# Performance work log

Measured on AMD Instinct MI355X. Metric: run time of the kernel, lower is better.

Reference implementation:

```python
import jax, jax.numpy as jnp
import numpy as np
import math

DMODEL = 1024
DFF = 4096
NUM_EXPERTS = 8
TOPK = 2
CAP_FACTOR = 1.25
EPS = 1.1920929e-07  # torch.finfo(float32).eps


def _trunc_normal(key, shape, fan_in, scale=1.0):
    std = scale * (1.0 / fan_in) ** 0.5
    return jax.random.truncated_normal(key, -2.0, 2.0, shape, jnp.float32) * std


def setup_inputs() -> dict:
    key = jax.random.key(0)
    ks = jax.random.split(key, 5)
    return {
        "x": jax.random.normal(ks[0], (2, 2048, DMODEL), jnp.float32),
        "router_weight": _trunc_normal(ks[1], (NUM_EXPERTS, DMODEL), DMODEL),
        "ff_pre_act_weight": _trunc_normal(ks[2], (NUM_EXPERTS, DFF, DMODEL), DMODEL),
        "gate_weight": _trunc_normal(ks[3], (NUM_EXPERTS, DFF, DMODEL), DMODEL),
        "ff_post_act_weight": _trunc_normal(ks[4], (NUM_EXPERTS, DMODEL, DFF), DFF),
    }


def reference(x, router_weight, ff_pre_act_weight, gate_weight, ff_post_act_weight):
    orig_shape = x.shape
    h = x.reshape(-1, DMODEL)                      # [T, d]
    T = h.shape[0]

    # ---- router: softmax + top-k, renormalize top-k probs ----
    logits = jnp.einsum('th,eh->te', h, router_weight)
    probs = jax.nn.softmax(logits.astype(jnp.float32), axis=-1)
    topk_probs, selected = jax.lax.top_k(probs, TOPK)          # [T,k]
    topk_probs = topk_probs / jnp.maximum(topk_probs.sum(-1, keepdims=True), EPS)

    flat_tokens = jnp.repeat(jnp.arange(T), TOPK)              # [T*k]
    flat_experts = selected.reshape(-1)
    flat_weights = topk_probs.reshape(-1)
    A = T * TOPK                                               # total assignments (static)
    capacity = max(1, math.ceil(CAP_FACTOR * A / NUM_EXPERTS))

    # ---- stable sort: by weight desc, then grouped by expert (stable) ----
    weight_order = jnp.argsort(-flat_weights, stable=True)
    grouped_order = jnp.argsort(flat_experts[weight_order], stable=True)
    sort_order = weight_order[grouped_order]
    se = flat_experts[sort_order]
    st = flat_tokens[sort_order]
    sw = flat_weights[sort_order]

    # ---- capacity dropping (mask instead of boolean filter, jit-safe) ----
    counts = jnp.bincount(se, length=NUM_EXPERTS)
    offsets = jnp.cumsum(counts) - counts
    slot = jnp.arange(A) - offsets[se]
    keep = slot < capacity
    sw = jnp.where(keep, sw, 0.0)

    # renormalize weights over kept assignments per token
    token_wsum = jnp.zeros(T, jnp.float32).at[st].add(sw)
    kept_w = sw / jnp.maximum(token_wsum[st], EPS)

    # ---- dispatch: scatter tokens into [E*capacity, d] (+1 dump row for dropped) ----
    FC = NUM_EXPERTS * capacity
    dispatch = jnp.where(keep, se * capacity + slot, FC)
    expert_inputs = jnp.zeros((FC + 1, DMODEL), x.dtype).at[dispatch].set(h[st])
    expert_inputs = expert_inputs[:FC].reshape(NUM_EXPERTS, capacity, DMODEL)

    # ---- grouped SwiGLU expert GEMMs ----
    pre = jnp.einsum('ech,edh->ecd', expert_inputs, ff_pre_act_weight)
    gate = jnp.einsum('ech,edh->ecd', expert_inputs, gate_weight)
    expert_out = jnp.einsum('ecd,ehd->ech', pre * jax.nn.silu(gate), ff_post_act_weight)

    # ---- combine: gather per-assignment output, weight, scatter-add to tokens ----
    eo_flat = jnp.concatenate(
        [expert_out.reshape(FC, DMODEL), jnp.zeros((1, DMODEL), x.dtype)], axis=0)
    updates = eo_flat[dispatch] * kept_w.astype(x.dtype)[:, None]
    out = jnp.zeros((T, DMODEL), x.dtype).at[st].add(updates)
    return out.reshape(orig_shape)
```

## Files before the change

### kernel.cpp

```cpp
#include <hip/hip_runtime.h>
#include <math.h>

#define DMODEL 1024
#define DFF    4096
#define NE     8
#define EPSF   1.1920929e-07f

typedef float f4    __attribute__((ext_vector_type(4)));
typedef float f32x4 __attribute__((ext_vector_type(4)));
typedef short s16x8 __attribute__((ext_vector_type(8)));
typedef unsigned short u16x4 __attribute__((ext_vector_type(4)));

__device__ inline unsigned short bf16_rne(float f) {
  unsigned int u = __float_as_uint(f);
  u += 0x7fffu + ((u >> 16) & 1u);
  return (unsigned short)(u >> 16);
}
__device__ inline float bf16_up(unsigned short h) {
  return __uint_as_float(((unsigned int)h) << 16);
}

__global__ void moe_init(int* __restrict__ used_count, int* __restrict__ row_tok, int n_row) {
  int i = blockIdx.x * blockDim.x + threadIdx.x;
  if (i < NE) used_count[i] = 0;
  for (int j = i; j < n_row; j += gridDim.x * blockDim.x) row_tok[j] = -1;
}

__global__ __launch_bounds__(256)
void moe_router(const float* __restrict__ x, const float* __restrict__ rw,
                int* __restrict__ assign_e, float* __restrict__ assign_w, int T) {
  int gw = (int)((blockIdx.x * blockDim.x + threadIdx.x) >> 6);
  int lane = threadIdx.x & 63;
  if (gw >= T) return;
  const float* h = x + (size_t)gw * DMODEL;
  float acc[NE];
#pragma unroll
  for (int e = 0; e < NE; ++e) acc[e] = 0.f;
  for (int i = lane; i < DMODEL; i += 64) {
    float hv = h[i];
#pragma unroll
    for (int e = 0; e < NE; ++e) acc[e] = fmaf(hv, rw[e * DMODEL + i], acc[e]);
  }
#pragma unroll
  for (int e = 0; e < NE; ++e) {
    float v = acc[e];
    for (int o = 32; o > 0; o >>= 1) v += __shfl_xor(v, o, 64);
    acc[e] = v;
  }
  if (lane == 0) {
    float mx = acc[0];
#pragma unroll
    for (int e = 1; e < NE; ++e) mx = fmaxf(mx, acc[e]);
    float p[NE];
    float s = 0.f;
#pragma unroll
    for (int e = 0; e < NE; ++e) { p[e] = expf(acc[e] - mx); s += p[e]; }
#pragma unroll
    for (int e = 0; e < NE; ++e) p[e] /= s;
    int e0 = 0;
#pragma unroll
    for (int e = 1; e < NE; ++e) if (p[e] > p[e0]) e0 = e;
    int e1 = (e0 == 0) ? 1 : 0;
#pragma unroll
    for (int e = 0; e < NE; ++e) { if (e != e0 && p[e] > p[e1]) e1 = e; }
    float w0 = p[e0], w1 = p[e1];
    float wsum = fmaxf(w0 + w1, EPSF);
    assign_e[2 * gw] = e0;
    assign_e[2 * gw + 1] = e1;
    assign_w[2 * gw] = w0 / wsum;
    assign_w[2 * gw + 1] = w1 / wsum;
  }
}

__global__ __launch_bounds__(256)
void moe_rank(const int* __restrict__ assign_e, const float* __restrict__ assign_w,
              int* __restrict__ assign_slot, int* __restrict__ row_tok,
              int* __restrict__ used_count, int A, int cap) {
  int gw = (int)((blockIdx.x * blockDim.x + threadIdx.x) >> 6);
  int lane = threadIdx.x & 63;
  if (gw >= A) return;
  int e = assign_e[gw];
  float w = assign_w[gw];
  int cnt = 0;
  for (int j = lane; j < A; j += 64) {
    int ej = assign_e[j];
    float wj = assign_w[j];
    if (ej == e && (wj > w || (wj == w && j < gw))) cnt++;
  }
  for (int o = 32; o > 0; o >>= 1) cnt += __shfl_xor(cnt, o, 64);
  if (lane == 0) {
    if (cnt < cap) {
      assign_slot[gw] = cnt;
      row_tok[e * cap + cnt] = gw >> 1;
      atomicAdd(used_count + e, 1);
    } else {
      assign_slot[gw] = -1;
    }
  }
}

__global__ __launch_bounds__(256)
void moe_split(const float* __restrict__ src, unsigned short* __restrict__ hi,
               unsigned short* __restrict__ lo, long n4) {
  long i = (long)blockIdx.x * 256 + threadIdx.x;
  long stride = (long)gridDim.x * 256;
  for (; i < n4; i += stride) {
    f4 v = ((const f4*)src)[i];
    u16x4 h, l;
#pragma unroll
    for (int j = 0; j < 4; ++j) {
      unsigned short hb = bf16_rne(v[j]);
      h[j] = hb;
      l[j] = bf16_rne(v[j] - bf16_up(hb));
    }
    ((u16x4*)hi)[i] = h;
    ((u16x4*)lo)[i] = l;
  }
}


__global__ __launch_bounds__(512, 2)
void moe_ffn1_mfma(const unsigned short* __restrict__ xh, const unsigned short* __restrict__ xl,
                   const unsigned short* __restrict__ wph, const unsigned short* __restrict__ wpl,
                   const unsigned short* __restrict__ wgh, const unsigned short* __restrict__ wgl,
                   const int* __restrict__ row_tok, const int* __restrict__ used_count,
                   unsigned short* __restrict__ midh, unsigned short* __restrict__ midl,
                   int e_base, int cap) {
  const int z = blockIdx.z;
  const int e = e_base + z;
  const int used = used_count[e];
  const int m0 = blockIdx.x * 128;
  if (m0 >= used) return;
  const int n0 = blockIdx.y * 128;

  __shared__ unsigned short lds[6 * 4096];

  const int tid = threadIdx.x;
  const int sr = tid >> 2;
  const int sc = (tid & 3) ^ ((tid >> 3) & 3);
  int arow = m0 + sr; if (arow >= cap) arow = cap - 1;
  int tokr = row_tok[e * cap + arow]; if (tokr < 0) tokr = 0;
  const unsigned short* gAh = xh + (size_t)tokr * DMODEL + sc * 8;
  const unsigned short* gAl = xl + (size_t)tokr * DMODEL + sc * 8;
  const size_t wrow = ((size_t)z * DFF + n0 + sr) * DMODEL + sc * 8;
  const unsigned short* gPh = wph + wrow;
  const unsigned short* gPl = wpl + wrow;
  const unsigned short* gGh = wgh + wrow;
  const unsigned short* gGl = wgl + wrow;

  const int lane = tid & 63;
  const int wid = tid >> 6;
  const int wm = wid >> 2;
  const int wn = wid & 3;
  const int lr = lane & 15;
  const int lg = lane >> 4;
  const int swz = (lr >> 1) & 3;
  const int aoff = (wm * 64 + lr) * 32 + ((lg ^ swz) * 8);
  const int boff = (wn * 32 + lr) * 32 + ((lg ^ swz) * 8);

  f32x4 accP[4][2] = {};
  f32x4 accG[4][2] = {};

  for (int kk = 0; kk < DMODEL; kk += 32) {
    s16x8 vAh = *(const s16x8*)(gAh + kk);
    s16x8 vAl = *(const s16x8*)(gAl + kk);
    s16x8 vPh = *(const s16x8*)(gPh + kk);
    s16x8 vPl = *(const s16x8*)(gPl + kk);
    s16x8 vGh = *(const s16x8*)(gGh + kk);
    s16x8 vGl = *(const s16x8*)(gGl + kk);
    __syncthreads();
    *(s16x8*)&lds[0 * 4096 + tid * 8] = vAh;
    *(s16x8*)&lds[1 * 4096 + tid * 8] = vAl;
    *(s16x8*)&lds[2 * 4096 + tid * 8] = vPh;
    *(s16x8*)&lds[3 * 4096 + tid * 8] = vPl;
    *(s16x8*)&lds[4 * 4096 + tid * 8] = vGh;
    *(s16x8*)&lds[5 * 4096 + tid * 8] = vGl;
    __syncthreads();
    s16x8 ah[4], al[4];
#pragma unroll
    for (int fm = 0; fm < 4; ++fm) {
      ah[fm] = *(const s16x8*)&lds[0 * 4096 + aoff + fm * 512];
      al[fm] = *(const s16x8*)&lds[1 * 4096 + aoff + fm * 512];
    }
#pragma unroll
    for (int fn = 0; fn < 2; ++fn) {
      s16x8 bh = *(const s16x8*)&lds[2 * 4096 + boff + fn * 512];
      s16x8 bl = *(const s16x8*)&lds[3 * 4096 + boff + fn * 512];
      s16x8 ch = *(const s16x8*)&lds[4 * 4096 + boff + fn * 512];
      s16x8 cl = *(const s16x8*)&lds[5 * 4096 + boff + fn * 512];
#pragma unroll
      for (int fm = 0; fm < 4; ++fm) {
        accP[fm][fn] = __builtin_amdgcn_mfma_f32_16x16x32_bf16(ah[fm], bh, accP[fm][fn], 0, 0, 0);
        accP[fm][fn] = __builtin_amdgcn_mfma_f32_16x16x32_bf16(ah[fm], bl, accP[fm][fn], 0, 0, 0);
        accP[fm][fn] = __builtin_amdgcn_mfma_f32_16x16x32_bf16(al[fm], bh, accP[fm][fn], 0, 0, 0);
        accG[fm][fn] = __builtin_amdgcn_mfma_f32_16x16x32_bf16(ah[fm], ch, accG[fm][fn], 0, 0, 0);
        accG[fm][fn] = __builtin_amdgcn_mfma_f32_16x16x32_bf16(ah[fm], cl, accG[fm][fn], 0, 0, 0);
        accG[fm][fn] = __builtin_amdgcn_mfma_f32_16x16x32_bf16(al[fm], ch, accG[fm][fn], 0, 0, 0);
      }
    }
  }

#pragma unroll
  for (int fm = 0; fm < 4; ++fm)
#pragma unroll
    for (int fn = 0; fn < 2; ++fn) {
      int m = m0 + wm * 64 + fm * 16 + lg * 4;
      int n = n0 + wn * 32 + fn * 16 + lr;
#pragma unroll
      for (int r = 0; r < 4; ++r) {
        if (m + r >= cap) continue;
        float gv = accG[fm][fn][r];
        float v = accP[fm][fn][r] * (gv / (1.f + expf(-gv)));
        size_t idx = ((size_t)z * cap + (m + r)) * DFF + n;
        unsigned short hb = bf16_rne(v);
        midh[idx] = hb;
        midl[idx] = bf16_rne(v - bf16_up(hb));
      }
    }
}

__global__ __launch_bounds__(512, 2)
void moe_ffn2_mfma(const unsigned short* __restrict__ midh, const unsigned short* __restrict__ midl,
                   const unsigned short* __restrict__ wh, const unsigned short* __restrict__ wl,
                   const int* __restrict__ used_count, float* __restrict__ eout,
                   int e_base, int cap) {
  const int z = blockIdx.z;
  const int e = e_base + z;
  const int used = used_count[e];
  const int m0 = blockIdx.x * 128;
  if (m0 >= used) return;
  const int n0 = blockIdx.y * 128;

  __shared__ unsigned short lds[4 * 4096];

  const int tid = threadIdx.x;
  const int sr = tid >> 2;
  const int sc = (tid & 3) ^ ((tid >> 3) & 3);
  int arow = m0 + sr; if (arow >= cap) arow = cap - 1;
  const unsigned short* gAh = midh + ((size_t)z * cap + arow) * DFF + sc * 8;
  const unsigned short* gAl = midl + ((size_t)z * cap + arow) * DFF + sc * 8;
  const size_t wrow = ((size_t)z * DMODEL + n0 + sr) * DFF + sc * 8;
  const unsigned short* gBh = wh + wrow;
  const unsigned short* gBl = wl + wrow;

  const int lane = tid & 63;
  const int wid = tid >> 6;
  const int wm = wid >> 2;
  const int wn = wid & 3;
  const int lr = lane & 15;
  const int lg = lane >> 4;
  const int swz = (lr >> 1) & 3;
  const int aoff = (wm * 64 + lr) * 32 + ((lg ^ swz) * 8);
  const int boff = (wn * 32 + lr) * 32 + ((lg ^ swz) * 8);

  f32x4 acc[4][2] = {};

  for (int kk = 0; kk < DFF; kk += 32) {
    s16x8 vAh = *(const s16x8*)(gAh + kk);
    s16x8 vAl = *(const s16x8*)(gAl + kk);
    s16x8 vBh = *(const s16x8*)(gBh + kk);
    s16x8 vBl = *(const s16x8*)(gBl + kk);
    __syncthreads();
    *(s16x8*)&lds[0 * 4096 + tid * 8] = vAh;
    *(s16x8*)&lds[1 * 4096 + tid * 8] = vAl;
    *(s16x8*)&lds[2 * 4096 + tid * 8] = vBh;
    *(s16x8*)&lds[3 * 4096 + tid * 8] = vBl;
    __syncthreads();
    s16x8 ah[4], al[4];
#pragma unroll
    for (int fm = 0; fm < 4; ++fm) {
      ah[fm] = *(const s16x8*)&lds[0 * 4096 + aoff + fm * 512];
      al[fm] = *(const s16x8*)&lds[1 * 4096 + aoff + fm * 512];
    }
#pragma unroll
    for (int fn = 0; fn < 2; ++fn) {
      s16x8 bh = *(const s16x8*)&lds[2 * 4096 + boff + fn * 512];
      s16x8 bl = *(const s16x8*)&lds[3 * 4096 + boff + fn * 512];
#pragma unroll
      for (int fm = 0; fm < 4; ++fm) {
        acc[fm][fn] = __builtin_amdgcn_mfma_f32_16x16x32_bf16(ah[fm], bh, acc[fm][fn], 0, 0, 0);
        acc[fm][fn] = __builtin_amdgcn_mfma_f32_16x16x32_bf16(ah[fm], bl, acc[fm][fn], 0, 0, 0);
        acc[fm][fn] = __builtin_amdgcn_mfma_f32_16x16x32_bf16(al[fm], bh, acc[fm][fn], 0, 0, 0);
      }
    }
  }

#pragma unroll
  for (int fm = 0; fm < 4; ++fm)
#pragma unroll
    for (int fn = 0; fn < 2; ++fn) {
      int m = m0 + wm * 64 + fm * 16 + lg * 4;
      int n = n0 + wn * 32 + fn * 16 + lr;
#pragma unroll
      for (int r = 0; r < 4; ++r) {
        if (m + r >= cap) continue;
        eout[((size_t)e * cap + (m + r)) * DMODEL + n] = acc[fm][fn][r];
      }
    }
}

__global__ __launch_bounds__(256)
void moe_combine(const float* __restrict__ eout, const int* __restrict__ assign_e,
                 const float* __restrict__ assign_w, const int* __restrict__ assign_slot,
                 float* __restrict__ out, int cap) {
  int t = blockIdx.x;
  int e0 = assign_e[2 * t], e1 = assign_e[2 * t + 1];
  float w0 = assign_w[2 * t], w1 = assign_w[2 * t + 1];
  int s0 = assign_slot[2 * t], s1 = assign_slot[2 * t + 1];
  float k0 = (s0 >= 0) ? w0 : 0.f;
  float k1 = (s1 >= 0) ? w1 : 0.f;
  float wsum = fmaxf(k0 + k1, EPSF);
  k0 /= wsum;
  k1 /= wsum;
  int i = threadIdx.x * 4;
  f4 v = {0.f, 0.f, 0.f, 0.f};
  if (s0 >= 0) v += k0 * *(const f4*)(eout + ((size_t)e0 * cap + s0) * DMODEL + i);
  if (s1 >= 0) v += k1 * *(const f4*)(eout + ((size_t)e1 * cap + s1) * DMODEL + i);
  *(f4*)(out + (size_t)t * DMODEL + i) = v;
}

extern "C" void kernel_launch(void* const* d_in, const int* in_sizes, int n_in,
                              void* d_out, int out_size, void* d_ws, size_t ws_size,
                              hipStream_t stream) {
  const float* x     = (const float*)d_in[0];
  const float* rw    = (const float*)d_in[1];
  const float* wpre  = (const float*)d_in[2];
  const float* wgate = (const float*)d_in[3];
  const float* wpost = (const float*)d_in[4];
  float* out = (float*)d_out;

  const int T = in_sizes[0] / DMODEL;
  const int A = T * 2;
  int cap = (int)ceil(1.25 * (double)A / NE);
  if (cap < 1) cap = 1;

  char* ws = (char*)d_ws;
  size_t off = 0;
  auto alloc = [&](size_t bytes) -> void* {
    void* p = ws + off;
    off += (bytes + 255) & ~(size_t)255;
    return p;
  };
  int*   assign_e    = (int*)alloc((size_t)A * 4);
  float* assign_w    = (float*)alloc((size_t)A * 4);
  int*   assign_slot = (int*)alloc((size_t)A * 4);
  int*   used_count  = (int*)alloc(NE * 4);
  int*   row_tok     = (int*)alloc((size_t)NE * cap * 4);
  float* eout        = (float*)alloc((size_t)NE * cap * DMODEL * 4);
  unsigned short* xh = (unsigned short*)alloc((size_t)T * DMODEL * 2);
  unsigned short* xl = (unsigned short*)alloc((size_t)T * DMODEL * 2);

  const size_t wPE = (size_t)DFF * DMODEL;
  auto al256 = [](size_t b) { return (b + 255) & ~(size_t)255; };
  int G = NE;
  while (G > 1) {
    size_t slab = al256((size_t)G * wPE * 2);
    size_t mids = al256((size_t)G * cap * DFF * 2);
    if (off + 4 * slab + 2 * mids + 65536 <= ws_size) break;
    G >>= 1;
  }
  unsigned short* sAh  = (unsigned short*)alloc((size_t)G * wPE * 2);
  unsigned short* sAl  = (unsigned short*)alloc((size_t)G * wPE * 2);
  unsigned short* sBh  = (unsigned short*)alloc((size_t)G * wPE * 2);
  unsigned short* sBl  = (unsigned short*)alloc((size_t)G * wPE * 2);
  unsigned short* midh = (unsigned short*)alloc((size_t)G * cap * DFF * 2);
  unsigned short* midl = (unsigned short*)alloc((size_t)G * cap * DFF * 2);

  const int n_row = NE * cap;
  moe_init<<<dim3((n_row + 255) / 256), dim3(256), 0, stream>>>(used_count, row_tok, n_row);
  moe_router<<<dim3((T + 3) / 4), dim3(256), 0, stream>>>(x, rw, assign_e, assign_w, T);
  moe_rank<<<dim3((A + 3) / 4), dim3(256), 0, stream>>>(assign_e, assign_w, assign_slot,
                                                        row_tok, used_count, A, cap);
  long xq = (long)T * DMODEL / 4;
  moe_split<<<dim3((unsigned)((xq + 255) / 256 > 2048 ? 2048 : (xq + 255) / 256)),
              dim3(256), 0, stream>>>(x, xh, xl, xq);

  const int mt = (cap + 127) / 128;
  for (int g0 = 0; g0 < NE; g0 += G) {
    long wq = (long)G * wPE / 4;
    moe_split<<<dim3(2048), dim3(256), 0, stream>>>(wpre + (size_t)g0 * wPE, sAh, sAl, wq);
    moe_split<<<dim3(2048), dim3(256), 0, stream>>>(wgate + (size_t)g0 * wPE, sBh, sBl, wq);
    moe_ffn1_mfma<<<dim3(mt, DFF / 128, G), dim3(512), 0, stream>>>(
        xh, xl, sAh, sAl, sBh, sBl, row_tok, used_count, midh, midl, g0, cap);
    moe_split<<<dim3(2048), dim3(256), 0, stream>>>(wpost + (size_t)g0 * wPE, sAh, sAl, wq);
    moe_ffn2_mfma<<<dim3(mt, DMODEL / 128, G), dim3(512), 0, stream>>>(
        midh, midl, sAh, sAl, used_count, eout, g0, cap);
  }
  moe_combine<<<dim3(T), dim3(256), 0, stream>>>(eout, assign_e, assign_w, assign_slot, out, cap);
}
```

Baseline: 1.539 ms.

## Remap GEMM blocks per XCD and prefetch next K-slice into registers

Flattens the FFN GEMM grids to 1D and decodes block ids so that consecutive M-tiles sharing a weight panel land on the same XCD, improving L2 reuse of weights. It also issues global loads for the next K-step before the barrier, overlapping memory latency with the MFMA work. This adds register pressure and assumes the block count divides evenly across the 8 XCDs.

```diff
diff --git a/kernel.cpp b/kernel.cpp
--- a/kernel.cpp
+++ b/kernel.cpp
@@ -18,6 +18,17 @@
 }
 __device__ inline float bf16_up(unsigned short h) {
   return __uint_as_float(((unsigned int)h) << 16);
+}
+
+__device__ inline void xcd_decode(int d, int nw, int mt, int ntiles,
+                                  int& bx, int& by, int& z) {
+  int S = nw >> 3;
+  int xcd = d & 7;
+  int slot = d >> 3;
+  int panel = xcd * (S / mt) + slot / mt;
+  bx = slot % mt;
+  by = panel % ntiles;
+  z = panel / ntiles;
 }
 
 __global__ void moe_init(int* __restrict__ used_count, int* __restrict__ row_tok, int n_row) {
@@ -125,13 +136,14 @@
                    const unsigned short* __restrict__ wgh, const unsigned short* __restrict__ wgl,
                    const int* __restrict__ row_tok, const int* __restrict__ used_count,
                    unsigned short* __restrict__ midh, unsigned short* __restrict__ midl,
-                   int e_base, int cap) {
-  const int z = blockIdx.z;
+                   int e_base, int cap, int mt) {
+  int bx, by, z;
+  xcd_decode(blockIdx.x, gridDim.x, mt, DFF / 128, bx, by, z);
   const int e = e_base + z;
   const int used = used_count[e];
-  const int m0 = blockIdx.x * 128;
+  const int m0 = bx * 128;
   if (m0 >= used) return;
-  const int n0 = blockIdx.y * 128;
+  const int n0 = by * 128;
 
   __shared__ unsigned short lds[6 * 4096];
 
@@ -161,13 +173,14 @@
   f32x4 accP[4][2] = {};
   f32x4 accG[4][2] = {};
 
+  s16x8 vAh = *(const s16x8*)(gAh);
+  s16x8 vAl = *(const s16x8*)(gAl);
+  s16x8 vPh = *(const s16x8*)(gPh);
+  s16x8 vPl = *(const s16x8*)(gPl);
+  s16x8 vGh = *(const s16x8*)(gGh);
+  s16x8 vGl = *(const s16x8*)(gGl);
+
   for (int kk = 0; kk < DMODEL; kk += 32) {
-    s16x8 vAh = *(const s16x8*)(gAh + kk);
-    s16x8 vAl = *(const s16x8*)(gAl + kk);
-    s16x8 vPh = *(const s16x8*)(gPh + kk);
-    s16x8 vPl = *(const s16x8*)(gPl + kk);
-    s16x8 vGh = *(const s16x8*)(gGh + kk);
-    s16x8 vGl = *(const s16x8*)(gGl + kk);
     __syncthreads();
     *(s16x8*)&lds[0 * 4096 + tid * 8] = vAh;
     *(s16x8*)&lds[1 * 4096 + tid * 8] = vAl;
@@ -175,6 +188,14 @@
     *(s16x8*)&lds[3 * 4096 + tid * 8] = vPl;
     *(s16x8*)&lds[4 * 4096 + tid * 8] = vGh;
     *(s16x8*)&lds[5 * 4096 + tid * 8] = vGl;
+    if (kk + 32 < DMODEL) {
+      vAh = *(const s16x8*)(gAh + kk + 32);
+      vAl = *(const s16x8*)(gAl + kk + 32);
+      vPh = *(const s16x8*)(gPh + kk + 32);
+      vPl = *(const s16x8*)(gPl + kk + 32);
+      vGh = *(const s16x8*)(gGh + kk + 32);
+      vGl = *(const s16x8*)(gGl + kk + 32);
+    }
     __syncthreads();
     s16x8 ah[4], al[4];
 #pragma unroll
@@ -223,13 +244,14 @@
 void moe_ffn2_mfma(const unsigned short* __restrict__ midh, const unsigned short* __restrict__ midl,
                    const unsigned short* __restrict__ wh, const unsigned short* __restrict__ wl,
                    const int* __restrict__ used_count, float* __restrict__ eout,
-                   int e_base, int cap) {
-  const int z = blockIdx.z;
+                   int e_base, int cap, int mt) {
+  int bx, by, z;
+  xcd_decode(blockIdx.x, gridDim.x, mt, DMODEL / 128, bx, by, z);
   const int e = e_base + z;
   const int used = used_count[e];
-  const int m0 = blockIdx.x * 128;
+  const int m0 = bx * 128;
   if (m0 >= used) return;
-  const int n0 = blockIdx.y * 128;
+  const int n0 = by * 128;
 
   __shared__ unsigned short lds[4 * 4096];
 
@@ -255,16 +277,23 @@
 
   f32x4 acc[4][2] = {};
 
+  s16x8 vAh = *(const s16x8*)(gAh);
+  s16x8 vAl = *(const s16x8*)(gAl);
+  s16x8 vBh = *(const s16x8*)(gBh);
+  s16x8 vBl = *(const s16x8*)(gBl);
+
   for (int kk = 0; kk < DFF; kk += 32) {
-    s16x8 vAh = *(const s16x8*)(gAh + kk);
-    s16x8 vAl = *(const s16x8*)(gAl + kk);
-    s16x8 vBh = *(const s16x8*)(gBh + kk);
-    s16x8 vBl = *(const s16x8*)(gBl + kk);
     __syncthreads();
     *(s16x8*)&lds[0 * 4096 + tid * 8] = vAh;
     *(s16x8*)&lds[1 * 4096 + tid * 8] = vAl;
     *(s16x8*)&lds[2 * 4096 + tid * 8] = vBh;
     *(s16x8*)&lds[3 * 4096 + tid * 8] = vBl;
+    if (kk + 32 < DFF) {
+      vAh = *(const s16x8*)(gAh + kk + 32);
+      vAl = *(const s16x8*)(gAl + kk + 32);
+      vBh = *(const s16x8*)(gBh + kk + 32);
+      vBl = *(const s16x8*)(gBl + kk + 32);
+    }
     __syncthreads();
     s16x8 ah[4], al[4];
 #pragma unroll
@@ -380,11 +409,11 @@
     long wq = (long)G * wPE / 4;
     moe_split<<<dim3(2048), dim3(256), 0, stream>>>(wpre + (size_t)g0 * wPE, sAh, sAl, wq);
     moe_split<<<dim3(2048), dim3(256), 0, stream>>>(wgate + (size_t)g0 * wPE, sBh, sBl, wq);
-    moe_ffn1_mfma<<<dim3(mt, DFF / 128, G), dim3(512), 0, stream>>>(
-        xh, xl, sAh, sAl, sBh, sBl, row_tok, used_count, midh, midl, g0, cap);
+    moe_ffn1_mfma<<<dim3(mt * (DFF / 128) * G), dim3(512), 0, stream>>>(
+        xh, xl, sAh, sAl, sBh, sBl, row_tok, used_count, midh, midl, g0, cap, mt);
     moe_split<<<dim3(2048), dim3(256), 0, stream>>>(wpost + (size_t)g0 * wPE, sAh, sAl, wq);
-    moe_ffn2_mfma<<<dim3(mt, DMODEL / 128, G), dim3(512), 0, stream>>>(
-        midh, midl, sAh, sAl, used_count, eout, g0, cap);
+    moe_ffn2_mfma<<<dim3(mt * (DMODEL / 128) * G), dim3(512), 0, stream>>>(
+        midh, midl, sAh, sAl, used_count, eout, g0, cap, mt);
   }
   moe_combine<<<dim3(T), dim3(256), 0, stream>>>(eout, assign_e, assign_w, assign_slot, out, cap);
 }
```

Result: faster. 1.333 ms (-13.4%).
